# Kernel tuning notes

Hardware: AMD Instinct MI355X
Metric: run time of the kernel (lower is better)

## Reference

```python
import jax, jax.numpy as jnp
import numpy as np

B, S, L, H, N_ITEMS = 16, 20, 64, 768, 50000  # sessions, max items/session, tokens/item, hidden, catalog
T = S * L
TEMP = 0.05       # config.temp
PAD_POS = 50      # pad item position id (see torch code)
EPS = 1e-8        # torch CosineSimilarity eps


def setup_inputs() -> dict:
    key = jax.random.key(0)
    k1, k2, k3, k4 = jax.random.split(key, 4)
    hidden = jax.random.normal(k1, (B, T, H), jnp.float32)
    emb = jax.random.normal(k2, (N_ITEMS, H), jnp.float32)
    # item position ids: each item's L tokens share position 1..S; padded items -> 50
    pos = np.tile(np.repeat(np.arange(1, S + 1), L)[None, :], (B, 1))  # [B,T]
    sess_len = np.asarray(jax.random.randint(k3, (B,), S // 2, S + 1))  # items per session
    item_idx = np.repeat(np.arange(S), L)[None, :]                      # [1,T]
    pos = np.where(item_idx < sess_len[:, None], pos, PAD_POS).astype(np.int32)
    attn = (pos != PAD_POS).astype(np.int32)
    attrs = np.asarray(jax.random.randint(k4, (B, T), 0, 4)).astype(np.int32)
    return {
        "hidden_states": hidden,
        "item_embedding": emb,
        "attention_mask": jnp.asarray(attn),
        "item_position_ids": jnp.asarray(pos),
        "attr_type_ids": jnp.asarray(attrs),
    }


def reference(hidden_states, item_embedding, attention_mask, item_position_ids, attr_type_ids):
    # --- RecformerPooler (pooler_type='item'): nan-mean pool tokens per item ---
    item_ids = jnp.arange(1, S + 1, dtype=item_position_ids.dtype)
    mask = item_position_ids[:, None, :] == item_ids[None, :, None]      # [B,S,T]
    counts = mask.sum(-1)                                                # [B,S]
    valid = counts > 0                                                   # items present in session
    maskf = mask.astype(hidden_states.dtype)
    pooled = jnp.einsum('bst,bth->bsh', maskf, hidden_states)
    pooled = pooled / jnp.maximum(counts, 1)[..., None].astype(hidden_states.dtype)
    # (torch produces NaN rows for invalid items; we carry `valid` instead)

    # --- Similarity: cosine / temp vs full item catalog ---
    pn = jnp.maximum(jnp.linalg.norm(pooled, axis=-1, keepdims=True), EPS)
    en = jnp.maximum(jnp.linalg.norm(item_embedding, axis=-1, keepdims=True), EPS)
    sim = jnp.einsum('bsh,nh->bns', pooled / pn, item_embedding / en) / TEMP  # [B,N,S]

    # --- reduce_session('maxsim'): NaN -> -inf, max over session items ---
    sim = jnp.where(valid[:, None, :], sim, -jnp.inf)
    scores = sim.max(axis=-1)  # [B, N]; trailing mean over attr dim (size 1) is identity
    return scores
```

## Files before the change

kernel.cpp:

```cpp
#include <hip/hip_runtime.h>

#define B_ 16
#define S_ 20
#define L_ 64
#define T_ 1280
#define H_ 768
#define NITEMS 50000
#define TEMP 0.05f
#define EPSN 1e-8f

#define BM 320
#define BN 128
#define BK 32
#define NKT (H_ / BK)

typedef __attribute__((ext_vector_type(8))) short short8;
typedef __attribute__((ext_vector_type(4))) short short4v;
typedef __attribute__((ext_vector_type(4))) float f32x4;

__device__ __forceinline__ unsigned short f2bf(float f) {
    unsigned int u = __float_as_uint(f);
    u = u + 0x7FFFu + ((u >> 16) & 1u);
    return (unsigned short)(u >> 16);
}

typedef __attribute__((address_space(3))) void lds_void;
typedef const __attribute__((address_space(1))) void gbl_void;
__device__ __forceinline__ void load_lds16(const void* g, void* l) {
    __builtin_amdgcn_global_load_lds((gbl_void*)g, (lds_void*)l, 16, 0, 0);
}

__global__ __launch_bounds__(192) void pool_kernel(const float* __restrict__ hidden,
                                                   const int* __restrict__ pos,
                                                   unsigned short* __restrict__ A,
                                                   int* __restrict__ valid) {
    const int row = blockIdx.x;
    const int b = row / S_, s = row % S_;
    const int tid = threadIdx.x;

    __shared__ float wgt[L_];
    __shared__ int cntS;
    __shared__ float red[3];

    const int* pbase = pos + b * T_ + s * L_;
    if (tid < L_) {
        const int match = (pbase[tid] == s + 1) ? 1 : 0;
        unsigned long long bal = __ballot(match);
        wgt[tid] = match ? 1.0f : 0.0f;
        if (tid == 0) cntS = (int)__popcll(bal);
    }
    __syncthreads();

    const int cnt = cntS;
    const float inv = 1.0f / (float)(cnt > 0 ? cnt : 1);
    const float* hbase = hidden + ((size_t)b * T_ + (size_t)s * L_) * H_ + tid * 4;

    float a0 = 0.f, a1 = 0.f, a2 = 0.f, a3 = 0.f;
#pragma unroll 8
    for (int t = 0; t < L_; ++t) {
        const float w = wgt[t];
        const float4 v = *reinterpret_cast<const float4*>(hbase + (size_t)t * H_);
        a0 += w * v.x; a1 += w * v.y; a2 += w * v.z; a3 += w * v.w;
    }
    a0 *= inv; a1 *= inv; a2 *= inv; a3 *= inv;

    float ss = a0 * a0 + a1 * a1 + a2 * a2 + a3 * a3;
#pragma unroll
    for (int off = 32; off; off >>= 1) ss += __shfl_xor(ss, off, 64);
    const int wave = tid >> 6, lane = tid & 63;
    if (lane == 0) red[wave] = ss;
    __syncthreads();
    const float tot = red[0] + red[1] + red[2];
    const float scale = 1.0f / (fmaxf(sqrtf(tot), EPSN) * TEMP);

    short4v w4;
    w4[0] = (short)f2bf(a0 * scale);
    w4[1] = (short)f2bf(a1 * scale);
    w4[2] = (short)f2bf(a2 * scale);
    w4[3] = (short)f2bf(a3 * scale);
    *reinterpret_cast<short4v*>(A + (size_t)row * H_ + tid * 4) = w4;
    if (tid == 0) valid[row] = (cnt > 0) ? 1 : 0;
}

__global__ __launch_bounds__(256, 2) void gemm_kernel(const float* __restrict__ emb,
                                                      const unsigned short* __restrict__ A,
                                                      const int* __restrict__ valid,
                                                      float* __restrict__ out) {
    const int n0 = blockIdx.x * BN;
    const int tid = threadIdx.x;
    const int wave = tid >> 6, lane = tid & 63, quad = lane >> 4, lq = lane & 15;

    __shared__ alignas(16) short As[2][BM * BK];
    __shared__ alignas(16) float Bs[2][BN * BK];
    __shared__ float sEn[BN];
    __shared__ int sMask[B_];

    if (tid < B_) {
        int m = 0;
        for (int s = 0; s < S_; ++s) m |= (valid[tid * S_ + s] ? 1 : 0) << s;
        sMask[tid] = m;
    }

    const unsigned short* aSrc = A + (size_t)(tid >> 2) * H_ + (tid & 3) * 8;
    const float* bSrc[4];
#pragma unroll
    for (int i = 0; i < 4; ++i) {
        int r = n0 + (tid >> 3) + i * 32;
        if (r > NITEMS - 1) r = NITEMS - 1;
        bSrc[i] = emb + (size_t)r * H_ + (tid & 7) * 4;
    }

#pragma unroll
    for (int i = 0; i < 5; ++i)
        load_lds16(aSrc + i * 64 * H_, (char*)(&As[0][0]) + tid * 16 + i * 4096);
#pragma unroll
    for (int i = 0; i < 4; ++i)
        load_lds16(bSrc[i], (char*)(&Bs[0][0]) + tid * 16 + i * 4096);

    float rowSq = 0.f;
    f32x4 acc[20][2];
#pragma unroll
    for (int i = 0; i < 20; ++i) {
        acc[i][0] = (f32x4)0.f;
        acc[i][1] = (f32x4)0.f;
    }

    int cur = 0;
    for (int kt = 0; kt < NKT; ++kt) {
        __syncthreads();
        if (kt + 1 < NKT) {
            const int k0 = (kt + 1) * BK;
#pragma unroll
            for (int i = 0; i < 5; ++i)
                load_lds16(aSrc + k0 + i * 64 * H_,
                           (char*)(&As[cur ^ 1][0]) + tid * 16 + i * 4096);
#pragma unroll
            for (int i = 0; i < 4; ++i)
                load_lds16(bSrc[i] + k0,
                           (char*)(&Bs[cur ^ 1][0]) + tid * 16 + i * 4096);
        }

        {
            const float* ep = &Bs[cur][(tid >> 1) * BK + (tid & 1) * 16];
#pragma unroll
            for (int i = 0; i < 4; ++i) {
                const float4 v = *reinterpret_cast<const float4*>(ep + i * 4);
                rowSq += v.x * v.x + v.y * v.y + v.z * v.z + v.w * v.w;
            }
        }

        short8 bF[2];
#pragma unroll
        for (int nf = 0; nf < 2; ++nf) {
            const float* bp = &Bs[cur][(wave * 32 + nf * 16 + lq) * BK + quad * 8];
            const float4 x = *reinterpret_cast<const float4*>(bp);
            const float4 y = *reinterpret_cast<const float4*>(bp + 4);
            short8 f;
            f[0] = (short)f2bf(x.x); f[1] = (short)f2bf(x.y);
            f[2] = (short)f2bf(x.z); f[3] = (short)f2bf(x.w);
            f[4] = (short)f2bf(y.x); f[5] = (short)f2bf(y.y);
            f[6] = (short)f2bf(y.z); f[7] = (short)f2bf(y.w);
            bF[nf] = f;
        }

#pragma unroll
        for (int mf = 0; mf < 20; ++mf) {
            const short8 aF =
                *reinterpret_cast<const short8*>(&As[cur][(mf * 16 + lq) * BK + quad * 8]);
            acc[mf][0] = __builtin_amdgcn_mfma_f32_16x16x32_bf16(aF, bF[0], acc[mf][0], 0, 0, 0);
            acc[mf][1] = __builtin_amdgcn_mfma_f32_16x16x32_bf16(aF, bF[1], acc[mf][1], 0, 0, 0);
        }
        cur ^= 1;
    }

    rowSq += __shfl_xor(rowSq, 1, 64);
    if (!(tid & 1)) sEn[tid >> 1] = fmaxf(sqrtf(rowSq), EPSN);
    __syncthreads();

#pragma unroll
    for (int nf = 0; nf < 2; ++nf) {
        const int ncol = wave * 32 + nf * 16 + lq;
        const int n = n0 + ncol;
        if (n >= NITEMS) continue;
        const float inv_en = 1.0f / sEn[ncol];
#pragma unroll
        for (int bb = 0; bb < B_; ++bb) {
            const int rLo = bb * S_;
            const int msk = sMask[bb];
            float lm = -__builtin_inff();
            const int mfLo = rLo >> 4;
            const int mfHi = (rLo + S_ - 1) >> 4;
#pragma unroll
            for (int mf = mfLo; mf <= mfHi; ++mf)
#pragma unroll
                for (int e = 0; e < 4; ++e) {
                    const int r = mf * 16 + quad * 4 + e;
                    const unsigned off = (unsigned)(r - rLo);
                    const bool ok = (off < (unsigned)S_) && ((msk >> off) & 1);
                    lm = ok ? fmaxf(lm, acc[mf][nf][e]) : lm;
                }
            lm = fmaxf(lm, __shfl_xor(lm, 16, 64));
            lm = fmaxf(lm, __shfl_xor(lm, 32, 64));
            if (quad == 0)
                out[(size_t)bb * NITEMS + n] = lm * inv_en;
        }
    }
}

extern "C" void kernel_launch(void* const* d_in, const int* in_sizes, int n_in,
                              void* d_out, int out_size, void* d_ws, size_t ws_size,
                              hipStream_t stream) {
    const float* hidden = (const float*)d_in[0];
    const float* emb    = (const float*)d_in[1];
    const int*   pos    = (const int*)d_in[3];
    float* out = (float*)d_out;

    unsigned short* Abf = (unsigned short*)d_ws;
    int* valid = (int*)((char*)d_ws + (size_t)320 * 768 * 2);

    pool_kernel<<<dim3(320), dim3(192), 0, stream>>>(hidden, pos, Abf, valid);
    gemm_kernel<<<dim3((NITEMS + BN - 1) / BN), dim3(256), 0, stream>>>(emb, Abf, valid, out);
}
```

Measured before the change: 300.7 us.

## Convert catalog tile to bf16 once on load, swizzle LDS, repartition waves over M

The embedding tile is now loaded through registers, converted to bf16 once, and stored to LDS with an XOR swizzle, so it is no longer kept as fp32 and reconverted by every wave. The pooled A matrix is written pre-swizzled so the direct global-to-LDS copies produce the same bank-conflict-free layout. Each wave now owns 80 rows (four sessions) against all 128 columns instead of 32 columns against all rows, which cuts the A fragment loads per wave and changes the max-reduction epilogue to match. In exchange, the B loads now pass through VGPRs and the conversion work sits in the main loop.

```diff
diff --git a/kernel.cpp b/kernel.cpp
--- a/kernel.cpp
+++ b/kernel.cpp
@@ -78,7 +78,9 @@
     w4[1] = (short)f2bf(a1 * scale);
     w4[2] = (short)f2bf(a2 * scale);
     w4[3] = (short)f2bf(a3 * scale);
-    *reinterpret_cast<short4v*>(A + (size_t)row * H_ + tid * 4) = w4;
+    const int slot = tid >> 1;
+    const int slotSw = (slot & ~3) | ((slot & 3) ^ (row & 3));
+    *reinterpret_cast<short4v*>(A + (size_t)row * H_ + slotSw * 8 + (tid & 1) * 4) = w4;
     if (tid == 0) valid[row] = (cnt > 0) ? 1 : 0;
 }
 
@@ -91,7 +93,7 @@
     const int wave = tid >> 6, lane = tid & 63, quad = lane >> 4, lq = lane & 15;
 
     __shared__ alignas(16) short As[2][BM * BK];
-    __shared__ alignas(16) float Bs[2][BN * BK];
+    __shared__ alignas(16) short Bs[2][BN * BK];
     __shared__ float sEn[BN];
     __shared__ int sMask[B_];
 
@@ -102,91 +104,118 @@
     }
 
     const unsigned short* aSrc = A + (size_t)(tid >> 2) * H_ + (tid & 3) * 8;
-    const float* bSrc[4];
-#pragma unroll
-    for (int i = 0; i < 4; ++i) {
-        int r = n0 + (tid >> 3) + i * 32;
-        if (r > NITEMS - 1) r = NITEMS - 1;
-        bSrc[i] = emb + (size_t)r * H_ + (tid & 7) * 4;
-    }
-
+    const int brLoc = tid >> 1;
+    int brGlb = n0 + brLoc;
+    if (brGlb > NITEMS - 1) brGlb = NITEMS - 1;
+    const float* bSrc = emb + (size_t)brGlb * H_ + (tid & 1) * 16;
+    const int bw0 = brLoc * BK + ((((tid & 1) * 2) + 0) ^ (brLoc & 3)) * 8;
+    const int bw1 = brLoc * BK + ((((tid & 1) * 2) + 1) ^ (brLoc & 3)) * 8;
+
+    float rowSq = 0.f;
+
+    {
+        const float4 v0 = *reinterpret_cast<const float4*>(bSrc);
+        const float4 v1 = *reinterpret_cast<const float4*>(bSrc + 4);
+        const float4 v2 = *reinterpret_cast<const float4*>(bSrc + 8);
+        const float4 v3 = *reinterpret_cast<const float4*>(bSrc + 12);
+#pragma unroll
+        for (int i = 0; i < 5; ++i)
+            load_lds16(aSrc + i * 64 * H_, (char*)(&As[0][0]) + tid * 16 + i * 4096);
+        rowSq += v0.x * v0.x + v0.y * v0.y + v0.z * v0.z + v0.w * v0.w;
+        rowSq += v1.x * v1.x + v1.y * v1.y + v1.z * v1.z + v1.w * v1.w;
+        rowSq += v2.x * v2.x + v2.y * v2.y + v2.z * v2.z + v2.w * v2.w;
+        rowSq += v3.x * v3.x + v3.y * v3.y + v3.z * v3.z + v3.w * v3.w;
+        short8 lo, hi;
+        lo[0] = (short)f2bf(v0.x); lo[1] = (short)f2bf(v0.y);
+        lo[2] = (short)f2bf(v0.z); lo[3] = (short)f2bf(v0.w);
+        lo[4] = (short)f2bf(v1.x); lo[5] = (short)f2bf(v1.y);
+        lo[6] = (short)f2bf(v1.z); lo[7] = (short)f2bf(v1.w);
+        hi[0] = (short)f2bf(v2.x); hi[1] = (short)f2bf(v2.y);
+        hi[2] = (short)f2bf(v2.z); hi[3] = (short)f2bf(v2.w);
+        hi[4] = (short)f2bf(v3.x); hi[5] = (short)f2bf(v3.y);
+        hi[6] = (short)f2bf(v3.z); hi[7] = (short)f2bf(v3.w);
+        *reinterpret_cast<short8*>(&Bs[0][bw0]) = lo;
+        *reinterpret_cast<short8*>(&Bs[0][bw1]) = hi;
+    }
+
+    f32x4 acc[5][8];
 #pragma unroll
     for (int i = 0; i < 5; ++i)
-        load_lds16(aSrc + i * 64 * H_, (char*)(&As[0][0]) + tid * 16 + i * 4096);
-#pragma unroll
-    for (int i = 0; i < 4; ++i)
-        load_lds16(bSrc[i], (char*)(&Bs[0][0]) + tid * 16 + i * 4096);
-
-    float rowSq = 0.f;
-    f32x4 acc[20][2];
-#pragma unroll
-    for (int i = 0; i < 20; ++i) {
-        acc[i][0] = (f32x4)0.f;
-        acc[i][1] = (f32x4)0.f;
-    }
+#pragma unroll
+        for (int j = 0; j < 8; ++j) acc[i][j] = (f32x4)0.f;
+
+    __syncthreads();
 
     int cur = 0;
     for (int kt = 0; kt < NKT; ++kt) {
-        __syncthreads();
-        if (kt + 1 < NKT) {
+        float4 v0, v1, v2, v3;
+        const bool more = (kt + 1 < NKT);
+        if (more) {
             const int k0 = (kt + 1) * BK;
+            v0 = *reinterpret_cast<const float4*>(bSrc + k0);
+            v1 = *reinterpret_cast<const float4*>(bSrc + k0 + 4);
+            v2 = *reinterpret_cast<const float4*>(bSrc + k0 + 8);
+            v3 = *reinterpret_cast<const float4*>(bSrc + k0 + 12);
 #pragma unroll
             for (int i = 0; i < 5; ++i)
                 load_lds16(aSrc + k0 + i * 64 * H_,
                            (char*)(&As[cur ^ 1][0]) + tid * 16 + i * 4096);
-#pragma unroll
-            for (int i = 0; i < 4; ++i)
-                load_lds16(bSrc[i] + k0,
-                           (char*)(&Bs[cur ^ 1][0]) + tid * 16 + i * 4096);
-        }
-
-        {
-            const float* ep = &Bs[cur][(tid >> 1) * BK + (tid & 1) * 16];
-#pragma unroll
-            for (int i = 0; i < 4; ++i) {
-                const float4 v = *reinterpret_cast<const float4*>(ep + i * 4);
-                rowSq += v.x * v.x + v.y * v.y + v.z * v.z + v.w * v.w;
-            }
-        }
-
-        short8 bF[2];
-#pragma unroll
-        for (int nf = 0; nf < 2; ++nf) {
-            const float* bp = &Bs[cur][(wave * 32 + nf * 16 + lq) * BK + quad * 8];
-            const float4 x = *reinterpret_cast<const float4*>(bp);
-            const float4 y = *reinterpret_cast<const float4*>(bp + 4);
-            short8 f;
-            f[0] = (short)f2bf(x.x); f[1] = (short)f2bf(x.y);
-            f[2] = (short)f2bf(x.z); f[3] = (short)f2bf(x.w);
-            f[4] = (short)f2bf(y.x); f[5] = (short)f2bf(y.y);
-            f[6] = (short)f2bf(y.z); f[7] = (short)f2bf(y.w);
-            bF[nf] = f;
-        }
-
-#pragma unroll
-        for (int mf = 0; mf < 20; ++mf) {
-            const short8 aF =
-                *reinterpret_cast<const short8*>(&As[cur][(mf * 16 + lq) * BK + quad * 8]);
-            acc[mf][0] = __builtin_amdgcn_mfma_f32_16x16x32_bf16(aF, bF[0], acc[mf][0], 0, 0, 0);
-            acc[mf][1] = __builtin_amdgcn_mfma_f32_16x16x32_bf16(aF, bF[1], acc[mf][1], 0, 0, 0);
-        }
+        }
+
+        short8 bF[8];
+#pragma unroll
+        for (int nf = 0; nf < 8; ++nf) {
+            const int rB = nf * 16 + lq;
+            bF[nf] = *reinterpret_cast<const short8*>(
+                &Bs[cur][rB * BK + ((quad ^ (lq & 3)) * 8)]);
+        }
+
+#pragma unroll
+        for (int mf = 0; mf < 5; ++mf) {
+            const int rA = wave * 80 + mf * 16 + lq;
+            const short8 aF = *reinterpret_cast<const short8*>(
+                &As[cur][rA * BK + ((quad ^ (lq & 3)) * 8)]);
+#pragma unroll
+            for (int nf = 0; nf < 8; ++nf)
+                acc[mf][nf] =
+                    __builtin_amdgcn_mfma_f32_16x16x32_bf16(aF, bF[nf], acc[mf][nf], 0, 0, 0);
+        }
+
+        if (more) {
+            rowSq += v0.x * v0.x + v0.y * v0.y + v0.z * v0.z + v0.w * v0.w;
+            rowSq += v1.x * v1.x + v1.y * v1.y + v1.z * v1.z + v1.w * v1.w;
+            rowSq += v2.x * v2.x + v2.y * v2.y + v2.z * v2.z + v2.w * v2.w;
+            rowSq += v3.x * v3.x + v3.y * v3.y + v3.z * v3.z + v3.w * v3.w;
+            short8 lo, hi;
+            lo[0] = (short)f2bf(v0.x); lo[1] = (short)f2bf(v0.y);
+            lo[2] = (short)f2bf(v0.z); lo[3] = (short)f2bf(v0.w);
+            lo[4] = (short)f2bf(v1.x); lo[5] = (short)f2bf(v1.y);
+            lo[6] = (short)f2bf(v1.z); lo[7] = (short)f2bf(v1.w);
+            hi[0] = (short)f2bf(v2.x); hi[1] = (short)f2bf(v2.y);
+            hi[2] = (short)f2bf(v2.z); hi[3] = (short)f2bf(v2.w);
+            hi[4] = (short)f2bf(v3.x); hi[5] = (short)f2bf(v3.y);
+            hi[6] = (short)f2bf(v3.z); hi[7] = (short)f2bf(v3.w);
+            *reinterpret_cast<short8*>(&Bs[cur ^ 1][bw0]) = lo;
+            *reinterpret_cast<short8*>(&Bs[cur ^ 1][bw1]) = hi;
+        }
+        __syncthreads();
         cur ^= 1;
     }
 
     rowSq += __shfl_xor(rowSq, 1, 64);
-    if (!(tid & 1)) sEn[tid >> 1] = fmaxf(sqrtf(rowSq), EPSN);
-    __syncthreads();
-
-#pragma unroll
-    for (int nf = 0; nf < 2; ++nf) {
-        const int ncol = wave * 32 + nf * 16 + lq;
+    if (!(tid & 1)) sEn[brLoc] = fmaxf(sqrtf(rowSq), EPSN);
+    __syncthreads();
+
+#pragma unroll
+    for (int nf = 0; nf < 8; ++nf) {
+        const int ncol = nf * 16 + lq;
         const int n = n0 + ncol;
-        if (n >= NITEMS) continue;
         const float inv_en = 1.0f / sEn[ncol];
 #pragma unroll
-        for (int bb = 0; bb < B_; ++bb) {
-            const int rLo = bb * S_;
+        for (int bl = 0; bl < 4; ++bl) {
+            const int bb = wave * 4 + bl;
             const int msk = sMask[bb];
+            const int rLo = bl * S_;
             float lm = -__builtin_inff();
             const int mfLo = rLo >> 4;
             const int mfHi = (rLo + S_ - 1) >> 4;
@@ -201,7 +230,7 @@
                 }
             lm = fmaxf(lm, __shfl_xor(lm, 16, 64));
             lm = fmaxf(lm, __shfl_xor(lm, 32, 64));
-            if (quad == 0)
+            if (quad == 0 && n < NITEMS)
                 out[(size_t)bb * NITEMS + n] = lm * inv_en;
         }
     }
```

After: 295.5 us. No clear change (-1.7%).
